# Optimization experiments

Hardware: AMD Instinct MI355X
Metric: run time of the kernel (lower is better)

Reference implementation:

```python
import jax, jax.numpy as jnp
import numpy as np

N_NODES = 50000
N_EDGES = 600000
IN_C, HID_C, OUT_C = 128, 128, 64
NUM_GRAPHS = 512


def sage_conv(x, src, dst, Wl, bl, Wr):
    """PyG SAGEConv (aggr='mean'): out = mean_{j->i} x_j @ Wl + bl + x_i @ Wr."""
    n = x.shape[0]
    msg = x[src]  # [E, d] gather
    agg = jax.ops.segment_sum(msg, dst, num_segments=n)
    deg = jax.ops.segment_sum(jnp.ones((src.shape[0], 1), x.dtype), dst, num_segments=n)
    agg = agg / jnp.maximum(deg, 1.0)
    return agg @ Wl + bl + x @ Wr


def setup_inputs() -> dict:
    key = jax.random.key(0)
    ks = jax.random.split(key, 12)
    x = jax.random.normal(ks[0], (N_NODES, IN_C), dtype=jnp.float32)
    edge_index = jax.random.randint(ks[1], (2, N_EDGES), 0, N_NODES, dtype=jnp.int32)
    cluster = jnp.sort(jax.random.randint(ks[2], (N_NODES,), 0, NUM_GRAPHS, dtype=jnp.int32))
    def lin(k, din, dout):
        s = 1.0 / np.sqrt(din)
        return (jax.random.uniform(k, (din, dout), jnp.float32, -s, s))
    return {
        "x": x, "edge_index": edge_index, "cluster": cluster,
        "Wl0": lin(ks[3], IN_C, HID_C), "bl0": jnp.zeros((HID_C,), jnp.float32), "Wr0": lin(ks[4], IN_C, HID_C),
        "Wl1": lin(ks[5], HID_C, HID_C), "bl1": jnp.zeros((HID_C,), jnp.float32), "Wr1": lin(ks[6], HID_C, HID_C),
        "Wl2": lin(ks[7], HID_C, OUT_C), "bl2": jnp.zeros((OUT_C,), jnp.float32), "Wr2": lin(ks[8], HID_C, OUT_C),
    }


def reference(x, edge_index, cluster, Wl0, bl0, Wr0, Wl1, bl1, Wr1, Wl2, bl2, Wr2):
    src, dst = edge_index[0], edge_index[1]
    out = None
    # hidden SAGEConv layers + relu (dropout inactive in eval)
    for Wl, bl, Wr in ((Wl0, bl0, Wr0), (Wl1, bl1, Wr1)):
        out = sage_conv(x, src, dst, Wl, bl, Wr)
        x = jax.nn.relu(out)
    # scatter-mean graph pooling over cluster ids
    gsum = jax.ops.segment_sum(x, cluster, num_segments=NUM_GRAPHS)
    gcnt = jax.ops.segment_sum(jnp.ones((x.shape[0], 1), x.dtype), cluster, num_segments=NUM_GRAPHS)
    g = gsum / jnp.maximum(gcnt, 1.0)
    # final conv + log-softmax over classes
    xf = sage_conv(x, src, dst, Wl2, bl2, Wr2)
    return (jax.nn.log_softmax(xf, axis=-1), out, g)
```

## Files before the change

kernel.cpp:

```cpp
#include <hip/hip_runtime.h>
#include <math.h>

#define NN 50000
#define NE 600000
#define NG 512

typedef unsigned int u32;
typedef unsigned short u16;

typedef __attribute__((ext_vector_type(8))) short bf16x8;
typedef __attribute__((ext_vector_type(4))) float f32x4;
typedef __attribute__((ext_vector_type(4))) unsigned int u32x4;

__device__ __forceinline__ float bf2f(u16 u) {
  return __uint_as_float(((u32)u) << 16);
}
__device__ __forceinline__ u16 f2bf(float f) {
  u32 u = __float_as_uint(f);
  u32 lsb = (u >> 16) & 1u;
  u += 0x7fffu + lsb;
  return (u16)(u >> 16);
}

__global__ __launch_bounds__(256)
void prep_k(const float* __restrict__ x, u32* __restrict__ xb,
            const int* __restrict__ ei, int* __restrict__ deg,
            const float* __restrict__ Wl0, const float* __restrict__ Wr0, u16* __restrict__ WbT0,
            const float* __restrict__ Wl1, const float* __restrict__ Wr1, u16* __restrict__ WbT1,
            const float* __restrict__ Wl2, u16* __restrict__ WlT2,
            const float* __restrict__ Wr2, u16* __restrict__ WrT2) {
  int b = blockIdx.x;
  int tid = threadIdx.x;
  if (b < 12500) {
    int t = b * 256 + tid;
    float2 v = ((const float2*)x)[t];
    xb[t] = (u32)f2bf(v.x) | ((u32)f2bf(v.y) << 16);
  } else if (b < 14844) {
    int e = (b - 12500) * 256 + tid;
    if (e < NE) atomicAdd(&deg[ei[NE + e]], 1);
  } else if (b < 15100) {
    bool w1 = (b >= 14972);
    int t = (b - (w1 ? 14972 : 14844)) * 256 + tid;
    int n = t >> 8;
    int k = t & 255;
    const float* Wl = w1 ? Wl1 : Wl0;
    const float* Wr = w1 ? Wr1 : Wr0;
    float v = (k < 128) ? Wl[k * 128 + n] : Wr[(k - 128) * 128 + n];
    int c = k >> 3, e = k & 7;
    u16* dst = w1 ? WbT1 : WbT0;
    dst[n * 256 + (((c ^ (n & 7)) << 3) | e)] = f2bf(v);
  } else {
    bool wr = (b >= 15132);
    int t = (b - (wr ? 15132 : 15100)) * 256 + tid;
    int n = t >> 7;
    int k = t & 127;
    const float* W = wr ? Wr2 : Wl2;
    float v = W[k * 64 + n];
    int c = k >> 3, e = k & 7;
    u16* dst = wr ? WrT2 : WlT2;
    dst[n * 128 + (((c ^ (n & 7)) << 3) | e)] = f2bf(v);
  }
}

__global__ __launch_bounds__(256)
void scan1_k(const int* __restrict__ deg, int* __restrict__ bsum) {
  __shared__ int s[256];
  int idx = blockIdx.x * 256 + threadIdx.x;
  int v = (idx < NN) ? deg[idx] : 0;
  s[threadIdx.x] = v;
  __syncthreads();
  for (int off = 128; off > 0; off >>= 1) {
    if (threadIdx.x < off) s[threadIdx.x] += s[threadIdx.x + off];
    __syncthreads();
  }
  if (threadIdx.x == 0) bsum[blockIdx.x] = s[0];
}

__global__ __launch_bounds__(256)
void scan2_k(const int* __restrict__ bsum, int* __restrict__ bofs, int* __restrict__ row_ptr) {
  __shared__ int s[256];
  int t = threadIdx.x;
  int v = (t < 196) ? bsum[t] : 0;
  s[t] = v;
  __syncthreads();
  for (int off = 1; off < 256; off <<= 1) {
    int add = (t >= off) ? s[t - off] : 0;
    __syncthreads();
    s[t] += add;
    __syncthreads();
  }
  if (t < 196) bofs[t] = s[t] - v;
  if (t == 0) row_ptr[NN] = NE;
}

__global__ __launch_bounds__(256)
void scan3_k(const int* __restrict__ deg, const int* __restrict__ bofs,
             int* __restrict__ row_ptr, int* __restrict__ cursor) {
  __shared__ int s[256];
  int idx = blockIdx.x * 256 + threadIdx.x;
  int t = threadIdx.x;
  int v = (idx < NN) ? deg[idx] : 0;
  s[t] = v;
  __syncthreads();
  for (int off = 1; off < 256; off <<= 1) {
    int add = (t >= off) ? s[t - off] : 0;
    __syncthreads();
    s[t] += add;
    __syncthreads();
  }
  if (idx < NN) {
    int p = bofs[blockIdx.x] + s[t] - v;
    row_ptr[idx] = p;
    cursor[idx] = p;
  }
}

__global__ __launch_bounds__(256)
void fill_k(const int* __restrict__ ei, int* __restrict__ cursor, int* __restrict__ perm) {
  int e = blockIdx.x * 256 + threadIdx.x;
  if (e >= NE) return;
  int pos = atomicAdd(&cursor[ei[NE + e]], 1);
  perm[pos] = ei[e];
}

__global__ __launch_bounds__(256)
void gather4_k(const u16* __restrict__ xb, const int* __restrict__ row_ptr,
               const int* __restrict__ perm, u16* __restrict__ aggb) {
  int wave = threadIdx.x >> 6;
  int lane = threadIdx.x & 63;
  int grp  = lane >> 4;
  int l16  = lane & 15;
  int n = (blockIdx.x * 4 + wave) * 4 + grp;
  int beg = row_ptr[n];
  int cnt = row_ptr[n + 1] - beg;
  int beg_s = min(beg, NE - 1);
  int last = max(cnt - 1, 0);
  int m = max(cnt, __shfl_xor(cnt, 16));
  int jmax = max(m, __shfl_xor(m, 32));
  float acc[8];
#pragma unroll
  for (int i = 0; i < 8; i++) acc[i] = 0.f;
  const u32x4* xv = (const u32x4*)xb;
  for (int base = 0; base < jmax; base += 8) {
    int idx[8];
#pragma unroll
    for (int j = 0; j < 8; j++) idx[j] = perm[beg_s + min(base + j, last)];
    u32x4 v[8];
#pragma unroll
    for (int j = 0; j < 8; j++) v[j] = xv[(size_t)idx[j] * 16 + l16];
#pragma unroll
    for (int j = 0; j < 8; j++) {
      bool live = (base + j) < cnt;
#pragma unroll
      for (int w = 0; w < 4; w++) {
        u32 u = v[j][w];
        acc[2 * w]     += live ? __uint_as_float(u << 16) : 0.f;
        acc[2 * w + 1] += live ? __uint_as_float(u & 0xffff0000u) : 0.f;
      }
    }
  }
  float inv = 1.0f / fmaxf((float)cnt, 1.0f);
  u32x4 o;
#pragma unroll
  for (int w = 0; w < 4; w++)
    o[w] = (u32)f2bf(acc[2 * w] * inv) | ((u32)f2bf(acc[2 * w + 1] * inv) << 16);
  ((u32x4*)aggb)[(size_t)n * 16 + l16] = o;
}

__global__ __launch_bounds__(256)
void gather8_k(const u16* __restrict__ yb, const int* __restrict__ row_ptr,
               const int* __restrict__ perm, u16* __restrict__ aggy) {
  int wave = threadIdx.x >> 6;
  int lane = threadIdx.x & 63;
  int grp  = lane >> 3;
  int li   = lane & 7;
  int n = (blockIdx.x * 4 + wave) * 8 + grp;
  int ns = min(n, NN - 1);
  int beg = row_ptr[ns];
  int cnt = row_ptr[ns + 1] - beg;
  int beg_s = min(beg, NE - 1);
  int last = max(cnt - 1, 0);
  int m = max(cnt, __shfl_xor(cnt, 8));
  m = max(m, __shfl_xor(m, 16));
  int jmax = max(m, __shfl_xor(m, 32));
  float acc[8];
#pragma unroll
  for (int i = 0; i < 8; i++) acc[i] = 0.f;
  const u32x4* xv = (const u32x4*)yb;
  for (int base = 0; base < jmax; base += 8) {
    int idx[8];
#pragma unroll
    for (int j = 0; j < 8; j++) idx[j] = perm[beg_s + min(base + j, last)];
    u32x4 v[8];
#pragma unroll
    for (int j = 0; j < 8; j++) v[j] = xv[(size_t)idx[j] * 8 + li];
#pragma unroll
    for (int j = 0; j < 8; j++) {
      bool live = (base + j) < cnt;
#pragma unroll
      for (int w = 0; w < 4; w++) {
        u32 u = v[j][w];
        acc[2 * w]     += live ? __uint_as_float(u << 16) : 0.f;
        acc[2 * w + 1] += live ? __uint_as_float(u & 0xffff0000u) : 0.f;
      }
    }
  }
  float inv = 1.0f / fmaxf((float)cnt, 1.0f);
  u32x4 o;
#pragma unroll
  for (int w = 0; w < 4; w++)
    o[w] = (u32)f2bf(acc[2 * w] * inv) | ((u32)f2bf(acc[2 * w + 1] * inv) << 16);
  if (n < NN) ((u32x4*)aggy)[(size_t)n * 8 + li] = o;
}

template<bool WRITE_PRE>
__global__ __launch_bounds__(256)
void sage_mfma_v2_k(const u16* __restrict__ aggb, const u16* __restrict__ xbin,
                    const u16* __restrict__ WbT, const float* __restrict__ bl,
                    u16* __restrict__ xb_out, float* __restrict__ out_pre) {
  __shared__ u16 wsh[128 * 256];
  int tid = threadIdx.x;
  {
    const u32x4* g = (const u32x4*)WbT;
    u32x4* l = (u32x4*)wsh;
#pragma unroll
    for (int i = 0; i < 16; i++)
      l[tid + i * 256] = g[tid + i * 256];
  }
  __syncthreads();

  int wave = tid >> 6;
  int lane = tid & 63;
  int quad = lane >> 4;
  int m16  = lane & 15;
  int r0 = blockIdx.x * 64 + wave * 16;

  int rowA = min(r0 + m16, NN - 1);
  const u16* pa = aggb + (size_t)rowA * 128 + quad * 8;
  const u16* px = xbin + (size_t)rowA * 128 + quad * 8;
  bf16x8 a[8];
#pragma unroll
  for (int j = 0; j < 4; j++) a[j]     = *(const bf16x8*)(pa + j * 32);
#pragma unroll
  for (int j = 0; j < 4; j++) a[4 + j] = *(const bf16x8*)(px + j * 32);

  f32x4 acc[8];
#pragma unroll
  for (int nt = 0; nt < 8; nt++) acc[nt] = (f32x4){0.f, 0.f, 0.f, 0.f};

  int swz = m16 & 7;
#pragma unroll
  for (int ks = 0; ks < 8; ks++) {
#pragma unroll
    for (int nt = 0; nt < 8; nt++) {
      const u16* bp = wsh + (nt * 16 + m16) * 256 + (((quad + ks * 4) ^ swz) << 3);
      bf16x8 b = *(const bf16x8*)bp;
      acc[nt] = __builtin_amdgcn_mfma_f32_16x16x32_bf16(a[ks], b, acc[nt], 0, 0, 0);
    }
  }

  float bv[8];
#pragma unroll
  for (int nt = 0; nt < 8; nt++) bv[nt] = bl[nt * 16 + m16];

  int rbase = r0 + quad * 4;
#pragma unroll
  for (int r = 0; r < 4; r++) {
    int row = rbase + r;
    if (row < NN) {
#pragma unroll
      for (int nt = 0; nt < 8; nt++) {
        int col = nt * 16 + m16;
        float v = acc[nt][r] + bv[nt];
        if (WRITE_PRE) out_pre[(size_t)row * 128 + col] = v;
        xb_out[(size_t)row * 128 + col] = f2bf(fmaxf(v, 0.f));
      }
    }
  }
}

__global__ __launch_bounds__(256)
void gemm64_k(const u16* __restrict__ xbin, const u16* __restrict__ WT,
              u16* __restrict__ yb) {
  __shared__ u16 wsh[64 * 128];
  int tid = threadIdx.x;
  {
    const u32x4* g = (const u32x4*)WT;
    u32x4* l = (u32x4*)wsh;
#pragma unroll
    for (int i = 0; i < 4; i++)
      l[tid + i * 256] = g[tid + i * 256];
  }
  __syncthreads();

  int wave = tid >> 6;
  int lane = tid & 63;
  int quad = lane >> 4;
  int m16  = lane & 15;
  int r0 = blockIdx.x * 64 + wave * 16;

  int rowA = min(r0 + m16, NN - 1);
  const u16* px = xbin + (size_t)rowA * 128 + quad * 8;
  bf16x8 a[4];
#pragma unroll
  for (int j = 0; j < 4; j++) a[j] = *(const bf16x8*)(px + j * 32);

  f32x4 acc[4];
#pragma unroll
  for (int nt = 0; nt < 4; nt++) acc[nt] = (f32x4){0.f, 0.f, 0.f, 0.f};

  int swz = m16 & 7;
#pragma unroll
  for (int ks = 0; ks < 4; ks++) {
#pragma unroll
    for (int nt = 0; nt < 4; nt++) {
      const u16* bp = wsh + (nt * 16 + m16) * 128 + (((ks * 4 + quad) ^ swz) << 3);
      bf16x8 b = *(const bf16x8*)bp;
      acc[nt] = __builtin_amdgcn_mfma_f32_16x16x32_bf16(a[ks], b, acc[nt], 0, 0, 0);
    }
  }

  int rbase = r0 + quad * 4;
#pragma unroll
  for (int r = 0; r < 4; r++) {
    int row = rbase + r;
    if (row < NN) {
#pragma unroll
      for (int nt = 0; nt < 4; nt++)
        yb[(size_t)row * 64 + nt * 16 + m16] = f2bf(acc[nt][r]);
    }
  }
}

__global__ __launch_bounds__(256)
void sage64f_k(const u16* __restrict__ aggy, const u16* __restrict__ xbin,
               const u16* __restrict__ WT, const float* __restrict__ bl,
               float* __restrict__ out) {
  __shared__ u16 wsh[64 * 128];
  int tid = threadIdx.x;
  {
    const u32x4* g = (const u32x4*)WT;
    u32x4* l = (u32x4*)wsh;
#pragma unroll
    for (int i = 0; i < 4; i++)
      l[tid + i * 256] = g[tid + i * 256];
  }
  __syncthreads();

  int wave = tid >> 6;
  int lane = tid & 63;
  int quad = lane >> 4;
  int m16  = lane & 15;
  int r0 = blockIdx.x * 64 + wave * 16;

  int rowA = min(r0 + m16, NN - 1);
  const u16* px = xbin + (size_t)rowA * 128 + quad * 8;
  bf16x8 a[4];
#pragma unroll
  for (int j = 0; j < 4; j++) a[j] = *(const bf16x8*)(px + j * 32);

  f32x4 acc[4];
#pragma unroll
  for (int nt = 0; nt < 4; nt++) acc[nt] = (f32x4){0.f, 0.f, 0.f, 0.f};

  int swz = m16 & 7;
#pragma unroll
  for (int ks = 0; ks < 4; ks++) {
#pragma unroll
    for (int nt = 0; nt < 4; nt++) {
      const u16* bp = wsh + (nt * 16 + m16) * 128 + (((ks * 4 + quad) ^ swz) << 3);
      bf16x8 b = *(const bf16x8*)bp;
      acc[nt] = __builtin_amdgcn_mfma_f32_16x16x32_bf16(a[ks], b, acc[nt], 0, 0, 0);
    }
  }

  float bv[4];
#pragma unroll
  for (int nt = 0; nt < 4; nt++) bv[nt] = bl[nt * 16 + m16];

  int rbase = r0 + quad * 4;
#pragma unroll
  for (int r = 0; r < 4; r++) {
    int row = rbase + r;
    int rs = min(row, NN - 1);
    float v0 = acc[0][r] + bv[0] + bf2f(aggy[(size_t)rs * 64 + m16]);
    float v1 = acc[1][r] + bv[1] + bf2f(aggy[(size_t)rs * 64 + 16 + m16]);
    float v2 = acc[2][r] + bv[2] + bf2f(aggy[(size_t)rs * 64 + 32 + m16]);
    float v3 = acc[3][r] + bv[3] + bf2f(aggy[(size_t)rs * 64 + 48 + m16]);
    float m = fmaxf(fmaxf(v0, v1), fmaxf(v2, v3));
#pragma unroll
    for (int mk = 1; mk <= 8; mk <<= 1) m = fmaxf(m, __shfl_xor(m, mk));
    float s = __expf(v0 - m) + __expf(v1 - m) + __expf(v2 - m) + __expf(v3 - m);
#pragma unroll
    for (int mk = 1; mk <= 8; mk <<= 1) s += __shfl_xor(s, mk);
    float ls = m + __logf(s);
    if (row < NN) {
      float* orow = out + (size_t)row * 64;
      orow[m16]      = v0 - ls;
      orow[16 + m16] = v1 - ls;
      orow[32 + m16] = v2 - ls;
      orow[48 + m16] = v3 - ls;
    }
  }
}

__global__ __launch_bounds__(256)
void pool_seg_k(const u16* __restrict__ xb, const int* __restrict__ cluster,
                float* __restrict__ g) {
  __shared__ float sh[256];
  int gid = blockIdx.x;
  int t = threadIdx.x;
  int ch = t & 127;
  int half = t >> 7;
  int lo = 0, hi = NN;
  while (lo < hi) { int mid = (lo + hi) >> 1; if (cluster[mid] < gid) lo = mid + 1; else hi = mid; }
  int beg = lo;
  hi = NN;
  while (lo < hi) { int mid = (lo + hi) >> 1; if (cluster[mid] < gid + 1) lo = mid + 1; else hi = mid; }
  int end = lo;
  float s0 = 0.f, s1 = 0.f;
  int n = beg + half;
  for (; n + 2 < end; n += 4) {
    s0 += bf2f(xb[(size_t)n * 128 + ch]);
    s1 += bf2f(xb[(size_t)(n + 2) * 128 + ch]);
  }
  if (n < end) s0 += bf2f(xb[(size_t)n * 128 + ch]);
  sh[t] = s0 + s1;
  __syncthreads();
  if (t < 128) {
    float s = sh[t] + sh[t + 128];
    g[gid * 128 + t] = s / fmaxf((float)(end - beg), 1.0f);
  }
}

extern "C" void kernel_launch(void* const* d_in, const int* in_sizes, int n_in,
                              void* d_out, int out_size, void* d_ws, size_t ws_size,
                              hipStream_t stream) {
  const float* x   = (const float*)d_in[0];
  const int*   ei  = (const int*)d_in[1];
  const int*   cl  = (const int*)d_in[2];
  const float* Wl0 = (const float*)d_in[3];
  const float* bl0 = (const float*)d_in[4];
  const float* Wr0 = (const float*)d_in[5];
  const float* Wl1 = (const float*)d_in[6];
  const float* bl1 = (const float*)d_in[7];
  const float* Wr1 = (const float*)d_in[8];
  const float* Wl2 = (const float*)d_in[9];
  const float* bl2 = (const float*)d_in[10];
  const float* Wr2 = (const float*)d_in[11];
  float* out = (float*)d_out;

  char* ws = (char*)d_ws;
  u16*   xb0     = (u16*)  (ws);
  u16*   xb1     = (u16*)  (ws + 12800000);
  u16*   xb2     = (u16*)  (ws + 25600000);
  u16*   aggb    = (u16*)  (ws + 38400000);
  u16*   y2      = aggb;
  u16*   aggy    = (u16*)  (ws + 38400000 + 6400000);
  u16*   WbT0    = (u16*)  (ws + 51200000);
  u16*   WbT1    = (u16*)  (ws + 51265536);
  u16*   WlT2    = (u16*)  (ws + 51331072);
  u16*   WrT2    = (u16*)  (ws + 51347456);
  int*   deg     = (int*)  (ws + 51363840);
  int*   row_ptr = (int*)  (ws + 51564032);
  int*   cursor  = (int*)  (ws + 51764736);
  int*   perm    = (int*)  (ws + 51964736);
  int*   bsum    = (int*)  (ws + 54364736);
  int*   bofs    = (int*)  (ws + 54365568);

  float* out_lsm = out;
  float* out_pre = out + 3200000;
  float* out_g   = out + 9600000;

  hipMemsetAsync(deg, 0, 200000, stream);
  prep_k<<<15164, 256, 0, stream>>>(x, (u32*)xb0, ei, deg,
                                    Wl0, Wr0, WbT0, Wl1, Wr1, WbT1,
                                    Wl2, WlT2, Wr2, WrT2);

  scan1_k<<<196, 256, 0, stream>>>(deg, bsum);
  scan2_k<<<1, 256, 0, stream>>>(bsum, bofs, row_ptr);
  scan3_k<<<196, 256, 0, stream>>>(deg, bofs, row_ptr, cursor);
  fill_k<<<2344, 256, 0, stream>>>(ei, cursor, perm);

  gather4_k<<<3125, 256, 0, stream>>>(xb0, row_ptr, perm, aggb);
  sage_mfma_v2_k<false><<<782, 256, 0, stream>>>(aggb, xb0, WbT0, bl0, xb1, nullptr);

  gather4_k<<<3125, 256, 0, stream>>>(xb1, row_ptr, perm, aggb);
  sage_mfma_v2_k<true><<<782, 256, 0, stream>>>(aggb, xb1, WbT1, bl1, xb2, out_pre);

  pool_seg_k<<<NG, 256, 0, stream>>>(xb2, cl, out_g);

  gemm64_k<<<782, 256, 0, stream>>>(xb2, WlT2, y2);
  gather8_k<<<1563, 256, 0, stream>>>(y2, row_ptr, perm, aggy);
  sage64f_k<<<782, 256, 0, stream>>>(aggy, xb2, WrT2, bl2, out_lsm);
}
```

Before: 281.7 us.

## Gather neighbor features in 8-bit float format and fuse pooling with final GEMM

Adds a custom 8-bit float encoding (sign plus 7-bit exponent/mantissa) for node features and the layer-2 projected features. The edge gathers read these byte-sized rows instead of bf16, which halves the random-access gather traffic. Pooling and the 64-wide GEMM are merged into one launch. The trade is lower precision in the aggregated means, with a risk of exceeding tolerance, plus extra quantized writes in prep and layer 0.

Result: slower. 322.9 us (+14.6%).

```diff
diff --git a/kernel.cpp b/kernel.cpp
--- a/kernel.cpp
+++ b/kernel.cpp
@@ -7,6 +7,7 @@
 
 typedef unsigned int u32;
 typedef unsigned short u16;
+typedef unsigned char u8;
 
 typedef __attribute__((ext_vector_type(8))) short bf16x8;
 typedef __attribute__((ext_vector_type(4))) float f32x4;
@@ -22,8 +23,25 @@
   return (u16)(u >> 16);
 }
 
-__global__ __launch_bounds__(256)
-void prep_k(const float* __restrict__ x, u32* __restrict__ xb,
+__device__ __forceinline__ u8 f2q(float f) {
+  u32 b = __float_as_uint(f);
+  u32 s = (b >> 24) & 0x80u;
+  u32 mag = b & 0x7fffffffu;
+  u32 lsb = (mag >> 20) & 1u;
+  mag += 0x7ffffu + lsb;
+  int t = (int)(mag >> 20) - 960;
+  u32 em = (t < 0) ? 0u : ((t > 0x7e) ? 0x7eu : (u32)t);
+  return (u8)(s | em);
+}
+__device__ __forceinline__ float q2f(u32 u, int k) {
+  u32 s8 = (u >> (8 * k)) & 0xffu;
+  u32 em = s8 & 0x7fu;
+  u32 bits = ((s8 & 0x80u) << 24) | ((em << 20) + 0x3c000000u);
+  return em ? __uint_as_float(bits) : 0.f;
+}
+
+__global__ __launch_bounds__(256)
+void prep_k(const float* __restrict__ x, u32* __restrict__ xb, u16* __restrict__ xq16,
             const int* __restrict__ ei, int* __restrict__ deg,
             const float* __restrict__ Wl0, const float* __restrict__ Wr0, u16* __restrict__ WbT0,
             const float* __restrict__ Wl1, const float* __restrict__ Wr1, u16* __restrict__ WbT1,
@@ -35,6 +53,7 @@
     int t = b * 256 + tid;
     float2 v = ((const float2*)x)[t];
     xb[t] = (u32)f2bf(v.x) | ((u32)f2bf(v.y) << 16);
+    xq16[t] = (u16)f2q(v.x) | ((u16)f2q(v.y) << 8);
   } else if (b < 14844) {
     int e = (b - 12500) * 256 + tid;
     if (e < NE) atomicAdd(&deg[ei[NE + e]], 1);
@@ -124,52 +143,8 @@
 }
 
 __global__ __launch_bounds__(256)
-void gather4_k(const u16* __restrict__ xb, const int* __restrict__ row_ptr,
+void gatherq_k(const u8* __restrict__ xq, const int* __restrict__ row_ptr,
                const int* __restrict__ perm, u16* __restrict__ aggb) {
-  int wave = threadIdx.x >> 6;
-  int lane = threadIdx.x & 63;
-  int grp  = lane >> 4;
-  int l16  = lane & 15;
-  int n = (blockIdx.x * 4 + wave) * 4 + grp;
-  int beg = row_ptr[n];
-  int cnt = row_ptr[n + 1] - beg;
-  int beg_s = min(beg, NE - 1);
-  int last = max(cnt - 1, 0);
-  int m = max(cnt, __shfl_xor(cnt, 16));
-  int jmax = max(m, __shfl_xor(m, 32));
-  float acc[8];
-#pragma unroll
-  for (int i = 0; i < 8; i++) acc[i] = 0.f;
-  const u32x4* xv = (const u32x4*)xb;
-  for (int base = 0; base < jmax; base += 8) {
-    int idx[8];
-#pragma unroll
-    for (int j = 0; j < 8; j++) idx[j] = perm[beg_s + min(base + j, last)];
-    u32x4 v[8];
-#pragma unroll
-    for (int j = 0; j < 8; j++) v[j] = xv[(size_t)idx[j] * 16 + l16];
-#pragma unroll
-    for (int j = 0; j < 8; j++) {
-      bool live = (base + j) < cnt;
-#pragma unroll
-      for (int w = 0; w < 4; w++) {
-        u32 u = v[j][w];
-        acc[2 * w]     += live ? __uint_as_float(u << 16) : 0.f;
-        acc[2 * w + 1] += live ? __uint_as_float(u & 0xffff0000u) : 0.f;
-      }
-    }
-  }
-  float inv = 1.0f / fmaxf((float)cnt, 1.0f);
-  u32x4 o;
-#pragma unroll
-  for (int w = 0; w < 4; w++)
-    o[w] = (u32)f2bf(acc[2 * w] * inv) | ((u32)f2bf(acc[2 * w + 1] * inv) << 16);
-  ((u32x4*)aggb)[(size_t)n * 16 + l16] = o;
-}
-
-__global__ __launch_bounds__(256)
-void gather8_k(const u16* __restrict__ yb, const int* __restrict__ row_ptr,
-               const int* __restrict__ perm, u16* __restrict__ aggy) {
   int wave = threadIdx.x >> 6;
   int lane = threadIdx.x & 63;
   int grp  = lane >> 3;
@@ -183,10 +158,10 @@
   int m = max(cnt, __shfl_xor(cnt, 8));
   m = max(m, __shfl_xor(m, 16));
   int jmax = max(m, __shfl_xor(m, 32));
-  float acc[8];
-#pragma unroll
-  for (int i = 0; i < 8; i++) acc[i] = 0.f;
-  const u32x4* xv = (const u32x4*)yb;
+  float acc[16];
+#pragma unroll
+  for (int i = 0; i < 16; i++) acc[i] = 0.f;
+  const u32x4* xv = (const u32x4*)xq;
   for (int base = 0; base < jmax; base += 8) {
     int idx[8];
 #pragma unroll
@@ -200,24 +175,86 @@
 #pragma unroll
       for (int w = 0; w < 4; w++) {
         u32 u = v[j][w];
-        acc[2 * w]     += live ? __uint_as_float(u << 16) : 0.f;
-        acc[2 * w + 1] += live ? __uint_as_float(u & 0xffff0000u) : 0.f;
+#pragma unroll
+        for (int k = 0; k < 4; k++) {
+          float f = q2f(u, k);
+          acc[w * 4 + k] += live ? f : 0.f;
+        }
       }
     }
   }
   float inv = 1.0f / fmaxf((float)cnt, 1.0f);
-  u32x4 o;
-#pragma unroll
-  for (int w = 0; w < 4; w++)
-    o[w] = (u32)f2bf(acc[2 * w] * inv) | ((u32)f2bf(acc[2 * w + 1] * inv) << 16);
-  if (n < NN) ((u32x4*)aggy)[(size_t)n * 8 + li] = o;
-}
-
-template<bool WRITE_PRE>
+  u32 o[8];
+#pragma unroll
+  for (int p = 0; p < 8; p++)
+    o[p] = (u32)f2bf(acc[2 * p] * inv) | ((u32)f2bf(acc[2 * p + 1] * inv) << 16);
+  if (n < NN) {
+    u32x4* dst = (u32x4*)(aggb + (size_t)n * 128);
+    dst[li * 2]     = (u32x4){o[0], o[1], o[2], o[3]};
+    dst[li * 2 + 1] = (u32x4){o[4], o[5], o[6], o[7]};
+  }
+}
+
+__global__ __launch_bounds__(256)
+void gatherq64_k(const u8* __restrict__ yq, const int* __restrict__ row_ptr,
+                 const int* __restrict__ perm, u16* __restrict__ aggy) {
+  int wave = threadIdx.x >> 6;
+  int lane = threadIdx.x & 63;
+  int grp  = lane >> 2;
+  int li   = lane & 3;
+  int n = (blockIdx.x * 4 + wave) * 16 + grp;
+  int ns = min(n, NN - 1);
+  int beg = row_ptr[ns];
+  int cnt = row_ptr[ns + 1] - beg;
+  int beg_s = min(beg, NE - 1);
+  int last = max(cnt - 1, 0);
+  int m = max(cnt, __shfl_xor(cnt, 4));
+  m = max(m, __shfl_xor(m, 8));
+  m = max(m, __shfl_xor(m, 16));
+  int jmax = max(m, __shfl_xor(m, 32));
+  float acc[16];
+#pragma unroll
+  for (int i = 0; i < 16; i++) acc[i] = 0.f;
+  const u32x4* xv = (const u32x4*)yq;
+  for (int base = 0; base < jmax; base += 8) {
+    int idx[8];
+#pragma unroll
+    for (int j = 0; j < 8; j++) idx[j] = perm[beg_s + min(base + j, last)];
+    u32x4 v[8];
+#pragma unroll
+    for (int j = 0; j < 8; j++) v[j] = xv[(size_t)idx[j] * 4 + li];
+#pragma unroll
+    for (int j = 0; j < 8; j++) {
+      bool live = (base + j) < cnt;
+#pragma unroll
+      for (int w = 0; w < 4; w++) {
+        u32 u = v[j][w];
+#pragma unroll
+        for (int k = 0; k < 4; k++) {
+          float f = q2f(u, k);
+          acc[w * 4 + k] += live ? f : 0.f;
+        }
+      }
+    }
+  }
+  float inv = 1.0f / fmaxf((float)cnt, 1.0f);
+  u32 o[8];
+#pragma unroll
+  for (int p = 0; p < 8; p++)
+    o[p] = (u32)f2bf(acc[2 * p] * inv) | ((u32)f2bf(acc[2 * p + 1] * inv) << 16);
+  if (n < NN) {
+    u32x4* dst = (u32x4*)(aggy + (size_t)n * 64);
+    dst[li * 2]     = (u32x4){o[0], o[1], o[2], o[3]};
+    dst[li * 2 + 1] = (u32x4){o[4], o[5], o[6], o[7]};
+  }
+}
+
+template<bool WRITE_PRE, bool WRITE_XQ>
 __global__ __launch_bounds__(256)
 void sage_mfma_v2_k(const u16* __restrict__ aggb, const u16* __restrict__ xbin,
                     const u16* __restrict__ WbT, const float* __restrict__ bl,
-                    u16* __restrict__ xb_out, float* __restrict__ out_pre) {
+                    u16* __restrict__ xb_out, float* __restrict__ out_pre,
+                    u8* __restrict__ xq_out) {
   __shared__ u16 wsh[128 * 256];
   int tid = threadIdx.x;
   {
@@ -273,23 +310,53 @@
         int col = nt * 16 + m16;
         float v = acc[nt][r] + bv[nt];
         if (WRITE_PRE) out_pre[(size_t)row * 128 + col] = v;
-        xb_out[(size_t)row * 128 + col] = f2bf(fmaxf(v, 0.f));
+        float rl = fmaxf(v, 0.f);
+        xb_out[(size_t)row * 128 + col] = f2bf(rl);
+        if (WRITE_XQ) xq_out[(size_t)row * 128 + col] = f2q(rl);
       }
     }
   }
 }
 
 __global__ __launch_bounds__(256)
-void gemm64_k(const u16* __restrict__ xbin, const u16* __restrict__ WT,
-              u16* __restrict__ yb) {
+void post_k(const u16* __restrict__ xb2, const int* __restrict__ cluster,
+            float* __restrict__ g, const u16* __restrict__ WlT2,
+            u8* __restrict__ yq) {
   __shared__ u16 wsh[64 * 128];
   int tid = threadIdx.x;
+  if (blockIdx.x < NG) {
+    float* sh = (float*)wsh;
+    int gid = blockIdx.x;
+    int ch = tid & 127;
+    int half = tid >> 7;
+    int lo = 0, hi = NN;
+    while (lo < hi) { int mid = (lo + hi) >> 1; if (cluster[mid] < gid) lo = mid + 1; else hi = mid; }
+    int beg = lo;
+    hi = NN;
+    while (lo < hi) { int mid = (lo + hi) >> 1; if (cluster[mid] < gid + 1) lo = mid + 1; else hi = mid; }
+    int end = lo;
+    float s0 = 0.f, s1 = 0.f;
+    int n = beg + half;
+    for (; n + 2 < end; n += 4) {
+      s0 += bf2f(xb2[(size_t)n * 128 + ch]);
+      s1 += bf2f(xb2[(size_t)(n + 2) * 128 + ch]);
+    }
+    if (n < end) s0 += bf2f(xb2[(size_t)n * 128 + ch]);
+    sh[tid] = s0 + s1;
+    __syncthreads();
+    if (tid < 128) {
+      float s = sh[tid] + sh[tid + 128];
+      g[gid * 128 + tid] = s / fmaxf((float)(end - beg), 1.0f);
+    }
+    return;
+  }
+  int bid = blockIdx.x - NG;
   {
-    const u32x4* g = (const u32x4*)WT;
+    const u32x4* gw = (const u32x4*)WlT2;
     u32x4* l = (u32x4*)wsh;
 #pragma unroll
     for (int i = 0; i < 4; i++)
-      l[tid + i * 256] = g[tid + i * 256];
+      l[tid + i * 256] = gw[tid + i * 256];
   }
   __syncthreads();
 
@@ -297,10 +364,10 @@
   int lane = tid & 63;
   int quad = lane >> 4;
   int m16  = lane & 15;
-  int r0 = blockIdx.x * 64 + wave * 16;
+  int r0 = bid * 64 + wave * 16;
 
   int rowA = min(r0 + m16, NN - 1);
-  const u16* px = xbin + (size_t)rowA * 128 + quad * 8;
+  const u16* px = xb2 + (size_t)rowA * 128 + quad * 8;
   bf16x8 a[4];
 #pragma unroll
   for (int j = 0; j < 4; j++) a[j] = *(const bf16x8*)(px + j * 32);
@@ -327,7 +394,7 @@
     if (row < NN) {
 #pragma unroll
       for (int nt = 0; nt < 4; nt++)
-        yb[(size_t)row * 64 + nt * 16 + m16] = f2bf(acc[nt][r]);
+        yq[(size_t)row * 64 + nt * 16 + m16] = f2q(acc[nt][r]);
     }
   }
 }
@@ -401,35 +468,6 @@
       orow[32 + m16] = v2 - ls;
       orow[48 + m16] = v3 - ls;
     }
-  }
-}
-
-__global__ __launch_bounds__(256)
-void pool_seg_k(const u16* __restrict__ xb, const int* __restrict__ cluster,
-                float* __restrict__ g) {
-  __shared__ float sh[256];
-  int gid = blockIdx.x;
-  int t = threadIdx.x;
-  int ch = t & 127;
-  int half = t >> 7;
-  int lo = 0, hi = NN;
-  while (lo < hi) { int mid = (lo + hi) >> 1; if (cluster[mid] < gid) lo = mid + 1; else hi = mid; }
-  int beg = lo;
-  hi = NN;
-  while (lo < hi) { int mid = (lo + hi) >> 1; if (cluster[mid] < gid + 1) lo = mid + 1; else hi = mid; }
-  int end = lo;
-  float s0 = 0.f, s1 = 0.f;
-  int n = beg + half;
-  for (; n + 2 < end; n += 4) {
-    s0 += bf2f(xb[(size_t)n * 128 + ch]);
-    s1 += bf2f(xb[(size_t)(n + 2) * 128 + ch]);
-  }
-  if (n < end) s0 += bf2f(xb[(size_t)n * 128 + ch]);
-  sh[t] = s0 + s1;
-  __syncthreads();
-  if (t < 128) {
-    float s = sh[t] + sh[t + 128];
-    g[gid * 128 + t] = s / fmaxf((float)(end - beg), 1.0f);
   }
 }
 
@@ -454,9 +492,10 @@
   u16*   xb0     = (u16*)  (ws);
   u16*   xb1     = (u16*)  (ws + 12800000);
   u16*   xb2     = (u16*)  (ws + 25600000);
+  u8*    xq      = (u8*)   (ws + 25600000);
   u16*   aggb    = (u16*)  (ws + 38400000);
-  u16*   y2      = aggb;
-  u16*   aggy    = (u16*)  (ws + 38400000 + 6400000);
+  u8*    y2q     = (u8*)   (ws + 38400000);
+  u16*   aggy    = (u16*)  (ws + 44800000);
   u16*   WbT0    = (u16*)  (ws + 51200000);
   u16*   WbT1    = (u16*)  (ws + 51265536);
   u16*   WlT2    = (u16*)  (ws + 51331072);
@@ -473,7 +512,7 @@
   float* out_g   = out + 9600000;
 
   hipMemsetAsync(deg, 0, 200000, stream);
-  prep_k<<<15164, 256, 0, stream>>>(x, (u32*)xb0, ei, deg,
+  prep_k<<<15164, 256, 0, stream>>>(x, (u32*)xb0, (u16*)xq, ei, deg,
                                     Wl0, Wr0, WbT0, Wl1, Wr1, WbT1,
                                     Wl2, WlT2, Wr2, WrT2);
 
@@ -482,15 +521,14 @@
   scan3_k<<<196, 256, 0, stream>>>(deg, bofs, row_ptr, cursor);
   fill_k<<<2344, 256, 0, stream>>>(ei, cursor, perm);
 
-  gather4_k<<<3125, 256, 0, stream>>>(xb0, row_ptr, perm, aggb);
-  sage_mfma_v2_k<false><<<782, 256, 0, stream>>>(aggb, xb0, WbT0, bl0, xb1, nullptr);
-
-  gather4_k<<<3125, 256, 0, stream>>>(xb1, row_ptr, perm, aggb);
-  sage_mfma_v2_k<true><<<782, 256, 0, stream>>>(aggb, xb1, WbT1, bl1, xb2, out_pre);
-
-  pool_seg_k<<<NG, 256, 0, stream>>>(xb2, cl, out_g);
-
-  gemm64_k<<<782, 256, 0, stream>>>(xb2, WlT2, y2);
-  gather8_k<<<1563, 256, 0, stream>>>(y2, row_ptr, perm, aggy);
+  gatherq_k<<<1563, 256, 0, stream>>>(xq, row_ptr, perm, aggb);
+  sage_mfma_v2_k<false, true><<<782, 256, 0, stream>>>(aggb, xb0, WbT0, bl0, xb1, nullptr, xq);
+
+  gatherq_k<<<1563, 256, 0, stream>>>(xq, row_ptr, perm, aggb);
+  sage_mfma_v2_k<true, false><<<782, 256, 0, stream>>>(aggb, xb1, WbT1, bl1, xb2, out_pre, nullptr);
+
+  post_k<<<NG + 782, 256, 0, stream>>>(xb2, cl, out_g, WlT2, y2q);
+
+  gatherq64_k<<<782, 256, 0, stream>>>(y2q, row_ptr, perm, aggy);
   sage64f_k<<<782, 256, 0, stream>>>(aggy, xb2, WrT2, bl2, out_lsm);
 }
```
